# Performance work log

Hardware: AMD Instinct MI355X
Metric: run time of the kernel (lower is better)

The kernel has to match this reference:

```python
import jax, jax.numpy as jnp
import numpy as np

N = 50000
E = 800000
NUM_GRAPHS = 128
X_IN, HID, EDGE_DIM = 64, 64, 16


def setup_inputs() -> dict:
    key = jax.random.key(0)
    ks = jax.random.split(key, 9)
    s = 0.05
    inp = {
        'x': jax.random.normal(ks[0], (N, X_IN), jnp.float32),
        'edge_index': jax.random.randint(ks[1], (2, E), 0, N, dtype=jnp.int32),
        'edge_attr': jax.random.normal(ks[2], (E, EDGE_DIM), jnp.float32),
        'batch': jnp.sort(jax.random.randint(ks[3], (N,), 0, NUM_GRAPHS, dtype=jnp.int32)),
        'w_fc1': jax.random.normal(ks[4], (EDGE_DIM, 1), jnp.float32) * s,
        'b_fc1': jnp.zeros((1,), jnp.float32),
    }
    dims = [(X_IN, HID), (HID, HID * 2), (HID * 2, HID)]
    for i, (din, dout) in enumerate(dims):
        k1, k2, k3 = jax.random.split(ks[5 + i], 3)
        inp[f'w1_{i}'] = jax.random.normal(k1, (din, dout), jnp.float32) * s
        inp[f'b1_{i}'] = jnp.zeros((dout,), jnp.float32)
        inp[f'w2_{i}'] = jax.random.normal(k2, (din, dout), jnp.float32) * s
        inp[f'w3_{i}'] = jax.random.normal(k3, (din, dout), jnp.float32) * s
        inp[f'b3_{i}'] = jnp.zeros((dout,), jnp.float32)
    return inp


def leconv(x, src, dst, ew, w1, b1, w2, w3, b3):
    # PyG LEConv: out_i = lin3(x_i) + sum_{j->i} e_ji * (lin1(x_j) - lin2(x_i))
    a = x @ w1 + b1          # lin1 (bias=True)   [N, out]
    b = x @ w2               # lin2 (bias=False)  [N, out]
    msg = ew[:, None] * (a[src] - b[dst])          # [E, out]
    agg = jax.ops.segment_sum(msg, dst, num_segments=N)
    return agg + x @ w3 + b3  # lin3 (bias=True)


def reference(x, edge_index, edge_attr, batch,
              w_fc1, b_fc1,
              w1_0, b1_0, w2_0, w3_0, b3_0,
              w1_1, b1_1, w2_1, w3_1, b3_1,
              w1_2, b1_2, w2_2, w3_2, b3_2):
    src, dst = edge_index[0], edge_index[1]
    ew = (edge_attr @ w_fc1 + b_fc1)[:, 0]         # fc1(edge_attr).squeeze(-1) -> [E]
    h = jax.nn.elu(leconv(x, src, dst, ew, w1_0, b1_0, w2_0, w3_0, b3_0))
    h = jax.nn.elu(leconv(h, src, dst, ew, w1_1, b1_1, w2_1, w3_1, b3_1))
    h = jax.nn.elu(leconv(h, src, dst, ew, w1_2, b1_2, w2_2, w3_2, b3_2))
    # global max pool over nodes of each graph -> [NUM_GRAPHS, HID]
    return jax.ops.segment_max(h, batch, num_segments=NUM_GRAPHS)
```

## Files before the change

### kernel.cpp

```cpp
#include <hip/hip_runtime.h>
#include <math.h>

#define N_NODES 50000
#define N_EDGES 800000
#define NUM_GRAPHS_ 128
#define SCAN_NB 98
#define NPASS 8
#define NODES_PER_PASS 6250
#define HCHUNKS 128
#define EDGES_PER_CHUNK 6250
#define HWORDS 12500

typedef unsigned short u16;
typedef unsigned int u32;
typedef __attribute__((ext_vector_type(8))) short bf16x8;
typedef __attribute__((ext_vector_type(4))) float f32x4;

__device__ __forceinline__ float elu_f(float v) {
    return v > 0.f ? v : (__expf(v) - 1.f);
}
__device__ __forceinline__ u16 f2bf(float f) {
    u32 u = __float_as_uint(f);
    u += 0x7FFFu + ((u >> 16) & 1u);
    return (u16)(u >> 16);
}
__device__ __forceinline__ float bf2f(u16 h) {
    return __uint_as_float(((u32)h) << 16);
}
__device__ __forceinline__ void bfpair(u32 v, float& lo, float& hi) {
    lo = __uint_as_float(v << 16);
    hi = __uint_as_float(v & 0xFFFF0000u);
}
__device__ __forceinline__ u32 packbf(float lo, float hi) {
    return (u32)f2bf(lo) | ((u32)f2bf(hi) << 16);
}

__global__ void conv_x_kernel(const float* __restrict__ x, u16* __restrict__ xb) {
    int g = blockIdx.x * blockDim.x + threadIdx.x;
    float4 v = ((const float4*)x)[g];
    uint2 o;
    o.x = packbf(v.x, v.y);
    o.y = packbf(v.z, v.w);
    ((uint2*)xb)[g] = o;
}

__global__ void ew_kernel(const float* __restrict__ edge_attr,
                          const float* __restrict__ w_fc1,
                          const float* __restrict__ b_fc1,
                          const int* __restrict__ edge_index,
                          float* __restrict__ ew,
                          u16* __restrict__ dst16) {
    int e = blockIdx.x * blockDim.x + threadIdx.x;
    if (e >= N_EDGES) return;
    const float4* ea = (const float4*)(edge_attr + (size_t)e * 16);
    const float4* wf = (const float4*)w_fc1;
    float acc = b_fc1[0];
#pragma unroll
    for (int i = 0; i < 4; i++) {
        float4 a = ea[i], w = wf[i];
        acc += a.x * w.x + a.y * w.y + a.z * w.z + a.w * w.w;
    }
    ew[e] = acc;
    dst16[e] = (u16)edge_index[N_EDGES + e];
}

__global__ __launch_bounds__(256) void deg_hist_kernel(const u16* __restrict__ dst16,
                                                       u32* __restrict__ partial) {
    __shared__ u32 bins[HWORDS];
    const int c = blockIdx.x >> 1;
    const int p = blockIdx.x & 1;
    const int t = threadIdx.x;
    for (int i = t; i < HWORDS; i += 256) bins[i] = 0;
    __syncthreads();
    const int base = c * EDGES_PER_CHUNK;
    const int nlo = p * 25000;
    for (int i = t; i < EDGES_PER_CHUNK; i += 256) {
        const int b = (int)dst16[base + i] - nlo;
        if ((unsigned)b < 25000u)
            atomicAdd(&bins[b >> 1], 1u << ((b & 1) * 16));
    }
    __syncthreads();
    u32* outp = partial + (size_t)blockIdx.x * HWORDS;
    for (int i = t; i < HWORDS; i += 256) outp[i] = bins[i];
}

__global__ __launch_bounds__(256) void scan_chunks_kernel(const u32* __restrict__ partial,
                                                          u32* __restrict__ prefpack,
                                                          u32* __restrict__ degpack) {
    const int g = blockIdx.x * 256 + threadIdx.x;
    if (g >= 25000) return;
    const int p = (g >= HWORDS) ? 1 : 0;
    const int wh = g - p * HWORDS;
    u32 runlo = 0, runhi = 0;
    for (int c = 0; c < HCHUNKS; c++) {
        prefpack[(size_t)c * 25000 + g] = runlo | (runhi << 16);
        u32 v = partial[(size_t)((c << 1) + p) * HWORDS + wh];
        runlo += v & 0xFFFFu;
        runhi += v >> 16;
    }
    degpack[g] = runlo | (runhi << 16);
}

__global__ __launch_bounds__(256) void scan1_kernel(const u32* __restrict__ degpack,
                                                    int* __restrict__ rowptr,
                                                    int* __restrict__ blk_sums) {
    __shared__ int sh[256];
    const int t = threadIdx.x;
    const int base = blockIdx.x * 512;
    const int i0 = base + 2 * t, i1 = i0 + 1;
    int d0 = 0, d1 = 0;
    if (i0 < N_NODES) {
        u32 v = degpack[i0 >> 1];
        d0 = (int)(v & 0xFFFFu);
        d1 = (int)(v >> 16);
    }
    const int pair = d0 + d1;
    int v = pair;
    sh[t] = v;
    __syncthreads();
#pragma unroll
    for (int off = 1; off < 256; off <<= 1) {
        int add = (t >= off) ? sh[t - off] : 0;
        __syncthreads();
        v += add;
        sh[t] = v;
        __syncthreads();
    }
    const int excl = v - pair;
    if (i0 < N_NODES) rowptr[i0] = excl;
    if (i1 < N_NODES) rowptr[i1] = excl + d0;
    if (t == 255) blk_sums[blockIdx.x] = v;
}

__global__ __launch_bounds__(128) void scan2_kernel(const int* __restrict__ blk_sums,
                                                    int* __restrict__ blk_offs,
                                                    int* __restrict__ rowptr) {
    __shared__ int sh[128];
    const int t = threadIdx.x;
    const int orig = (t < SCAN_NB) ? blk_sums[t] : 0;
    int v = orig;
    sh[t] = v;
    __syncthreads();
#pragma unroll
    for (int off = 1; off < 128; off <<= 1) {
        int add = (t >= off) ? sh[t - off] : 0;
        __syncthreads();
        v += add;
        sh[t] = v;
        __syncthreads();
    }
    if (t < SCAN_NB) blk_offs[t] = v - orig;
    if (t == 127) rowptr[N_NODES] = v;
}

__global__ void scan3_kernel(int* __restrict__ rowptr,
                             const int* __restrict__ blk_offs) {
    int i = blockIdx.x * blockDim.x + threadIdx.x;
    if (i >= N_NODES) return;
    rowptr[i] += blk_offs[i >> 9];
}

__global__ __launch_bounds__(256) void place_kernel(const int* __restrict__ edge_index,
                                                    const float* __restrict__ ew,
                                                    const u16* __restrict__ dst16,
                                                    const int* __restrict__ rowptr,
                                                    const u32* __restrict__ prefpack,
                                                    int2* __restrict__ csr) {
    __shared__ int lcur[NODES_PER_PASS];
    const int pass = blockIdx.x & (NPASS - 1);
    const int c = blockIdx.x >> 3;
    const int lo = pass * NODES_PER_PASS;
    const int t = threadIdx.x;
    for (int i = t; i < NODES_PER_PASS; i += 256) lcur[i] = 0;
    __syncthreads();
    const int base = c * EDGES_PER_CHUNK;
    for (int i = t; i < EDGES_PER_CHUNK; i += 256) {
        const int e = base + i;
        const int d = (int)dst16[e];
        const int dl = d - lo;
        if ((unsigned)dl < (unsigned)NODES_PER_PASS) {
            u32 pw = prefpack[(size_t)c * 25000 + (d >> 1)];
            int pref = (int)((pw >> ((d & 1) * 16)) & 0xFFFFu);
            int lpos = atomicAdd(&lcur[dl], 1);
            int2 ent;
            ent.x = edge_index[e];
            ent.y = __float_as_int(ew[e]);
            csr[rowptr[d] + pref + lpos] = ent;
        }
    }
}

template <int DIN, bool WRITE_C>
__global__ __launch_bounds__(256) void gather_kernel(
    const u16* __restrict__ xb, const int* __restrict__ rowptr,
    const int2* __restrict__ csr, u16* __restrict__ sb,
    u16* __restrict__ chb, float* __restrict__ c) {
    constexpr int CG = DIN / 4;
    constexpr int EG = 64 / CG;
    const int gid = blockIdx.x * 256 + threadIdx.x;
    const int node = gid >> 6;
    if (node >= N_NODES) return;
    const int lane = threadIdx.x & 63;
    const int cg = lane & (CG - 1);
    const int eg = lane / CG;
    const int beg = rowptr[node];
    const int end = rowptr[node + 1];
    const uint2* x2 = (const uint2*)xb;

    float a0 = 0.f, a1 = 0.f, a2 = 0.f, a3 = 0.f;
    float b0 = 0.f, b1 = 0.f, b2 = 0.f, b3 = 0.f;
    float wsum = 0.f;

    int p = beg + eg;
    for (; p + EG < end; p += 2 * EG) {
        int2 e0 = csr[p];
        int2 e1 = csr[p + EG];
        float w0 = __int_as_float(e0.y);
        float w1 = __int_as_float(e1.y);
        uint2 v0 = x2[(size_t)e0.x * CG + cg];
        uint2 v1 = x2[(size_t)e1.x * CG + cg];
        float f0, f1, f2, f3, g0, g1, g2, g3;
        bfpair(v0.x, f0, f1); bfpair(v0.y, f2, f3);
        bfpair(v1.x, g0, g1); bfpair(v1.y, g2, g3);
        a0 += w0 * f0; a1 += w0 * f1; a2 += w0 * f2; a3 += w0 * f3;
        b0 += w1 * g0; b1 += w1 * g1; b2 += w1 * g2; b3 += w1 * g3;
        wsum += w0 + w1;
    }
    if (p < end) {
        int2 e0 = csr[p];
        float w0 = __int_as_float(e0.y);
        uint2 v0 = x2[(size_t)e0.x * CG + cg];
        float f0, f1, f2, f3;
        bfpair(v0.x, f0, f1); bfpair(v0.y, f2, f3);
        a0 += w0 * f0; a1 += w0 * f1; a2 += w0 * f2; a3 += w0 * f3;
        wsum += w0;
    }
    a0 += b0; a1 += b1; a2 += b2; a3 += b3;

#pragma unroll
    for (int off = 32; off >= CG; off >>= 1) {
        a0 += __shfl_xor(a0, off);
        a1 += __shfl_xor(a1, off);
        a2 += __shfl_xor(a2, off);
        a3 += __shfl_xor(a3, off);
        wsum += __shfl_xor(wsum, off);
    }

    if (lane < CG) {
        uint2 so;
        so.x = packbf(a0, a1);
        so.y = packbf(a2, a3);
        ((uint2*)sb)[(size_t)node * CG + cg] = so;
        const float cn = WRITE_C ? wsum : c[node];
        uint2 hv = x2[(size_t)node * CG + cg];
        float h0, h1, h2, h3;
        bfpair(hv.x, h0, h1); bfpair(hv.y, h2, h3);
        uint2 co;
        co.x = packbf(cn * h0, cn * h1);
        co.y = packbf(cn * h2, cn * h3);
        ((uint2*)chb)[(size_t)node * CG + cg] = co;
    }
    if (WRITE_C && lane == 0) c[node] = wsum;
}

__global__ void pack_w_kernel(const float* __restrict__ w3_0, const float* __restrict__ w1_0, const float* __restrict__ w2_0,
                              const float* __restrict__ w3_1, const float* __restrict__ w1_1, const float* __restrict__ w2_1,
                              const float* __restrict__ w3_2, const float* __restrict__ w1_2, const float* __restrict__ w2_2,
                              u16* __restrict__ bp0, u16* __restrict__ bp1, u16* __restrict__ bp2) {
    int t = blockIdx.x * blockDim.x + threadIdx.x;
    if (t >= 7680) return;
    u16 buf[8];
    if (t < 4608) {
        int DIN, DOUT, lid;
        const float *w3, *w1, *w2;
        u16* bp;
        if (t < 1536) { DIN = 64; DOUT = 64;  lid = t;        w3 = w3_0; w1 = w1_0; w2 = w2_0; bp = bp0; }
        else          { DIN = 64; DOUT = 128; lid = t - 1536; w3 = w3_1; w1 = w1_1; w2 = w2_1; bp = bp1; }
        const int NT = DOUT / 16;
        const int lane = lid & 63;
        const int fragid = lid >> 6;
        const int chunk = fragid / NT;
        const int ntile = fragid % NT;
        const int n = ntile * 16 + (lane & 15);
        const int kbase = chunk * 32 + (lane >> 4) * 8;
#pragma unroll
        for (int j = 0; j < 8; j++) {
            int k = kbase + j;
            int region = k / DIN;
            int kk = k - region * DIN;
            float v = (region == 0) ? w3[kk * DOUT + n]
                    : (region == 1) ? w1[kk * DOUT + n]
                                    : -w2[kk * DOUT + n];
            buf[j] = f2bf(v);
        }
        *(bf16x8*)(bp + ((size_t)lid << 3)) = *(bf16x8*)buf;
    } else {
        const int lid = t - 4608;
        const int NT = 12;
        const int lane = lid & 63;
        const int fragid = lid >> 6;
        const int chunk = fragid / NT;
        const int ntile = fragid % NT;
        const int n = ntile * 16 + (lane & 15);
        const int kbase = chunk * 32 + (lane >> 4) * 8;
#pragma unroll
        for (int j = 0; j < 8; j++) {
            int k = kbase + j;
            float v = (n < 64)  ? w3_2[k * 64 + n]
                    : (n < 128) ? -w2_2[k * 64 + (n - 64)]
                                : w1_2[k * 64 + (n - 128)];
            buf[j] = f2bf(v);
        }
        *(bf16x8*)(bp2 + ((size_t)lid << 3)) = *(bf16x8*)buf;
    }
}

template <int DIN, int DOUT>
__global__ __launch_bounds__(256) void gemm_mfma(
    const u16* __restrict__ hb, const u16* __restrict__ sb,
    const u16* __restrict__ chb, const u16* __restrict__ Bp,
    const float* __restrict__ cvec, const float* __restrict__ bias1,
    const float* __restrict__ bias3, u16* __restrict__ outp) {
    constexpr int CH = DIN / 32;
    constexpr int CHUNKS = 3 * CH;
    constexpr int NT = DOUT / 16;
    const int tid = threadIdx.x;
    const int wv = tid >> 6;
    const int lane = tid & 63;
    const int l15 = lane & 15;
    const int q = lane >> 4;
    const int mhalf = wv & 1;
    const int nhalf = wv >> 1;
    const int row_base = blockIdx.x * 64 + mhalf * 32;
    const int nt0 = blockIdx.y * 4 + nhalf * 2;

    const int r0 = min(row_base + l15, N_NODES - 1);
    const int r1 = min(row_base + 16 + l15, N_NODES - 1);
    const int qo = q * 8;

    f32x4 acc00 = {0.f, 0.f, 0.f, 0.f};
    f32x4 acc01 = {0.f, 0.f, 0.f, 0.f};
    f32x4 acc10 = {0.f, 0.f, 0.f, 0.f};
    f32x4 acc11 = {0.f, 0.f, 0.f, 0.f};

#pragma unroll
    for (int chunk = 0; chunk < CHUNKS; chunk++) {
        const int region = chunk / CH;
        const int koff = (chunk - region * CH) * 32 + qo;
        const u16* A = (region == 0) ? hb : (region == 1) ? sb : chb;
        bf16x8 a0 = *(const bf16x8*)(A + (size_t)r0 * DIN + koff);
        bf16x8 a1 = *(const bf16x8*)(A + (size_t)r1 * DIN + koff);
        const u16* bp = Bp + (((size_t)(chunk * NT + nt0) * 64 + lane) << 3);
        bf16x8 bf0 = *(const bf16x8*)bp;
        bf16x8 bf1 = *(const bf16x8*)(bp + 64 * 8);
        acc00 = __builtin_amdgcn_mfma_f32_16x16x32_bf16(a0, bf0, acc00, 0, 0, 0);
        acc01 = __builtin_amdgcn_mfma_f32_16x16x32_bf16(a0, bf1, acc01, 0, 0, 0);
        acc10 = __builtin_amdgcn_mfma_f32_16x16x32_bf16(a1, bf0, acc10, 0, 0, 0);
        acc11 = __builtin_amdgcn_mfma_f32_16x16x32_bf16(a1, bf1, acc11, 0, 0, 0);
    }

#pragma unroll
    for (int ni = 0; ni < 2; ni++) {
        const int col = (nt0 + ni) * 16 + l15;
        const float B3 = bias3[col];
        const float B1 = bias1[col];
        const f32x4 am0 = ni ? acc01 : acc00;
        const f32x4 am1 = ni ? acc11 : acc10;
#pragma unroll
        for (int mi = 0; mi < 2; mi++) {
            const f32x4 av = mi ? am1 : am0;
#pragma unroll
            for (int reg = 0; reg < 4; reg++) {
                const int row = row_base + mi * 16 + q * 4 + reg;
                if (row < N_NODES) {
                    const float cv = cvec[row];
                    const float val = av[reg] + B3 + cv * B1;
                    outp[(size_t)row * DOUT + col] = f2bf(elu_f(val));
                }
            }
        }
    }
}

__global__ __launch_bounds__(256) void gemm_wide_kernel(
    const u16* __restrict__ hb, const u16* __restrict__ Bp,
    u16* __restrict__ zuy) {
    constexpr int NT = 12;
    const int tid = threadIdx.x;
    const int wv = tid >> 6;
    const int lane = tid & 63;
    const int l15 = lane & 15;
    const int q = lane >> 4;
    const int row_base = blockIdx.x * 64 + (wv & 1) * 32;
    const int nt0 = blockIdx.y * 4 + (wv >> 1) * 2;

    const int r0 = min(row_base + l15, N_NODES - 1);
    const int r1 = min(row_base + 16 + l15, N_NODES - 1);
    const int qo = q * 8;

    f32x4 acc00 = {0.f, 0.f, 0.f, 0.f};
    f32x4 acc01 = {0.f, 0.f, 0.f, 0.f};
    f32x4 acc10 = {0.f, 0.f, 0.f, 0.f};
    f32x4 acc11 = {0.f, 0.f, 0.f, 0.f};

#pragma unroll
    for (int chunk = 0; chunk < 4; chunk++) {
        const int koff = chunk * 32 + qo;
        bf16x8 a0 = *(const bf16x8*)(hb + (size_t)r0 * 128 + koff);
        bf16x8 a1 = *(const bf16x8*)(hb + (size_t)r1 * 128 + koff);
        const u16* bp = Bp + (((size_t)(chunk * NT + nt0) * 64 + lane) << 3);
        bf16x8 bf0 = *(const bf16x8*)bp;
        bf16x8 bf1 = *(const bf16x8*)(bp + 64 * 8);
        acc00 = __builtin_amdgcn_mfma_f32_16x16x32_bf16(a0, bf0, acc00, 0, 0, 0);
        acc01 = __builtin_amdgcn_mfma_f32_16x16x32_bf16(a0, bf1, acc01, 0, 0, 0);
        acc10 = __builtin_amdgcn_mfma_f32_16x16x32_bf16(a1, bf0, acc10, 0, 0, 0);
        acc11 = __builtin_amdgcn_mfma_f32_16x16x32_bf16(a1, bf1, acc11, 0, 0, 0);
    }

#pragma unroll
    for (int ni = 0; ni < 2; ni++) {
        const int col = (nt0 + ni) * 16 + l15;
        const f32x4 am0 = ni ? acc01 : acc00;
        const f32x4 am1 = ni ? acc11 : acc10;
#pragma unroll
        for (int mi = 0; mi < 2; mi++) {
            const f32x4 av = mi ? am1 : am0;
#pragma unroll
            for (int reg = 0; reg < 4; reg++) {
                const int row = row_base + mi * 16 + q * 4 + reg;
                if (row < N_NODES)
                    zuy[(size_t)row * 192 + col] = f2bf(av[reg]);
            }
        }
    }
}

__global__ __launch_bounds__(256) void gather2_kernel(
    const u16* __restrict__ zuy, const int* __restrict__ rowptr,
    const int2* __restrict__ csr, const float* __restrict__ c,
    const float* __restrict__ bias1, const float* __restrict__ bias3,
    u16* __restrict__ h3) {
    constexpr int CG = 16, EG = 4;
    const int gid = blockIdx.x * 256 + threadIdx.x;
    const int node = gid >> 6;
    if (node >= N_NODES) return;
    const int lane = threadIdx.x & 63;
    const int cg = lane & (CG - 1);
    const int eg = lane >> 4;
    const int beg = rowptr[node];
    const int end = rowptr[node + 1];

    float a0 = 0.f, a1 = 0.f, a2 = 0.f, a3 = 0.f;
    float b0 = 0.f, b1 = 0.f, b2 = 0.f, b3 = 0.f;

    int p = beg + eg;
    for (; p + EG < end; p += 2 * EG) {
        int2 e0 = csr[p];
        int2 e1 = csr[p + EG];
        float w0 = __int_as_float(e0.y);
        float w1 = __int_as_float(e1.y);
        uint2 v0 = ((const uint2*)(zuy + (size_t)e0.x * 192 + 128))[cg];
        uint2 v1 = ((const uint2*)(zuy + (size_t)e1.x * 192 + 128))[cg];
        float f0, f1, f2, f3, g0, g1, g2, g3;
        bfpair(v0.x, f0, f1); bfpair(v0.y, f2, f3);
        bfpair(v1.x, g0, g1); bfpair(v1.y, g2, g3);
        a0 += w0 * f0; a1 += w0 * f1; a2 += w0 * f2; a3 += w0 * f3;
        b0 += w1 * g0; b1 += w1 * g1; b2 += w1 * g2; b3 += w1 * g3;
    }
    if (p < end) {
        int2 e0 = csr[p];
        float w0 = __int_as_float(e0.y);
        uint2 v0 = ((const uint2*)(zuy + (size_t)e0.x * 192 + 128))[cg];
        float f0, f1, f2, f3;
        bfpair(v0.x, f0, f1); bfpair(v0.y, f2, f3);
        a0 += w0 * f0; a1 += w0 * f1; a2 += w0 * f2; a3 += w0 * f3;
    }
    a0 += b0; a1 += b1; a2 += b2; a3 += b3;

#pragma unroll
    for (int off = 32; off >= CG; off >>= 1) {
        a0 += __shfl_xor(a0, off);
        a1 += __shfl_xor(a1, off);
        a2 += __shfl_xor(a2, off);
        a3 += __shfl_xor(a3, off);
    }

    if (lane < CG) {
        const float cn = c[node];
        const u16* zr = zuy + (size_t)node * 192;
        uint2 zv = ((const uint2*)zr)[cg];
        uint2 uv = ((const uint2*)(zr + 64))[cg];
        float z0, z1, z2, z3, u0, u1, u2, u3;
        bfpair(zv.x, z0, z1); bfpair(zv.y, z2, z3);
        bfpair(uv.x, u0, u1); bfpair(uv.y, u2, u3);
        const float4 b3v = *(const float4*)(bias3 + cg * 4);
        const float4 b1v = *(const float4*)(bias1 + cg * 4);
        float o0 = elu_f(z0 + cn * u0 + a0 + b3v.x + cn * b1v.x);
        float o1 = elu_f(z1 + cn * u1 + a1 + b3v.y + cn * b1v.y);
        float o2 = elu_f(z2 + cn * u2 + a2 + b3v.z + cn * b1v.z);
        float o3 = elu_f(z3 + cn * u3 + a3 + b3v.w + cn * b1v.w);
        uint2 o;
        o.x = packbf(o0, o1);
        o.y = packbf(o2, o3);
        ((uint2*)h3)[(size_t)node * CG + cg] = o;
    }
}

__global__ void pool_kernel(const u16* __restrict__ h,
                            const int* __restrict__ batch,
                            float* __restrict__ out) {
    const int g = blockIdx.x;
    const int tid = threadIdx.x;
    int lo = 0, hi = N_NODES;
    while (lo < hi) { int mid = (lo + hi) >> 1; if (batch[mid] < g) lo = mid + 1; else hi = mid; }
    const int beg = lo;
    lo = beg; hi = N_NODES;
    while (lo < hi) { int mid = (lo + hi) >> 1; if (batch[mid] < g + 1) lo = mid + 1; else hi = mid; }
    const int end = lo;

    __shared__ float red[256];
    const int col = tid & 63;
    const int rg = tid >> 6;
    float m = -3.0e38f;
    for (int r = beg + rg; r < end; r += 4) m = fmaxf(m, bf2f(h[(size_t)r * 64 + col]));
    red[tid] = m;
    __syncthreads();
    if (tid < 64) {
        m = fmaxf(fmaxf(red[tid], red[tid + 64]), fmaxf(red[tid + 128], red[tid + 192]));
        out[g * 64 + tid] = m;
    }
}

extern "C" void kernel_launch(void* const* d_in, const int* in_sizes, int n_in,
                              void* d_out, int out_size, void* d_ws, size_t ws_size,
                              hipStream_t stream) {
    const float* x = (const float*)d_in[0];
    const int* ei = (const int*)d_in[1];
    const float* ea = (const float*)d_in[2];
    const int* batch = (const int*)d_in[3];
    const float* wfc = (const float*)d_in[4];
    const float* bfc = (const float*)d_in[5];
    const float* w1_0 = (const float*)d_in[6];
    const float* b1_0 = (const float*)d_in[7];
    const float* w2_0 = (const float*)d_in[8];
    const float* w3_0 = (const float*)d_in[9];
    const float* b3_0 = (const float*)d_in[10];
    const float* w1_1 = (const float*)d_in[11];
    const float* b1_1 = (const float*)d_in[12];
    const float* w2_1 = (const float*)d_in[13];
    const float* w3_1 = (const float*)d_in[14];
    const float* b3_1 = (const float*)d_in[15];
    const float* w1_2 = (const float*)d_in[16];
    const float* b1_2 = (const float*)d_in[17];
    const float* w2_2 = (const float*)d_in[18];
    const float* w3_2 = (const float*)d_in[19];
    const float* b3_2 = (const float*)d_in[20];
    float* out = (float*)d_out;

    char* ws = (char*)d_ws;
    float* ew      = (float*)(ws);
    float* c       = (float*)(ws + 3200000);
    int*   rowptr  = (int*)  (ws + 3800000);
    int2*  csr     = (int2*) (ws + 4000128);
    u16*   xb      = (u16*)  (ws + 10400128);
    u16*   sb      = (u16*)  (ws + 16800128);
    u16*   chb     = (u16*)  (ws + 29600128);
    u16*   h1      = (u16*)  (ws + 42400128);
    u16*   h2      = (u16*)  (ws + 48800128);
    u16*   h3      = (u16*)  (ws + 61600128);
    u16*   bp0     = (u16*)  (ws + 68000128);
    u16*   bp1     = (u16*)  (ws + 68024704);
    u16*   bp2     = (u16*)  (ws + 68073856);
    int* blk_sums  = (int*)  (ws + 68123008);
    int* blk_offs  = (int*)  (ws + 68123520);
    u16* dst16   = chb;
    u32* degpack = (u32*)(ws + 31600128);
    u32* partial = (u32*)sb;
    u32* prefpack = (u32*)h2;
    u16* zuy     = sb;

    conv_x_kernel<<<3125, 256, 0, stream>>>(x, xb);
    ew_kernel<<<(N_EDGES + 255) / 256, 256, 0, stream>>>(ea, wfc, bfc, ei, ew, dst16);
    pack_w_kernel<<<30, 256, 0, stream>>>(w3_0, w1_0, w2_0, w3_1, w1_1, w2_1,
                                          w3_2, w1_2, w2_2, bp0, bp1, bp2);
    deg_hist_kernel<<<HCHUNKS * 2, 256, 0, stream>>>(dst16, partial);
    scan_chunks_kernel<<<98, 256, 0, stream>>>(partial, prefpack, degpack);
    scan1_kernel<<<SCAN_NB, 256, 0, stream>>>(degpack, rowptr, blk_sums);
    scan2_kernel<<<1, 128, 0, stream>>>(blk_sums, blk_offs, rowptr);
    scan3_kernel<<<(N_NODES + 255) / 256, 256, 0, stream>>>(rowptr, blk_offs);
    place_kernel<<<HCHUNKS * NPASS, 256, 0, stream>>>(ei, ew, dst16, rowptr, prefpack, csr);

    const int RB = (N_NODES + 63) / 64;
    const int GBLK = (N_NODES * 64 + 255) / 256;

    gather_kernel<64, true><<<GBLK, 256, 0, stream>>>(xb, rowptr, csr, sb, chb, c);
    gemm_mfma<64, 64><<<dim3(RB, 1), 256, 0, stream>>>(xb, sb, chb, bp0, c, b1_0, b3_0, h1);

    gather_kernel<64, false><<<GBLK, 256, 0, stream>>>(h1, rowptr, csr, sb, chb, c);
    gemm_mfma<64, 128><<<dim3(RB, 2), 256, 0, stream>>>(h1, sb, chb, bp1, c, b1_1, b3_1, h2);

    gemm_wide_kernel<<<dim3(RB, 3), 256, 0, stream>>>(h2, bp2, zuy);
    gather2_kernel<<<GBLK, 256, 0, stream>>>(zuy, rowptr, csr, c, b1_2, b3_2, h3);

    pool_kernel<<<NUM_GRAPHS_, 256, 0, stream>>>(h3, batch, out);
}
```

Before: 350.0 us.

## Replace deterministic chunked CSR build with global-atomic degree count and placement

Replaces the shared-memory chunked histogram, multi-stage scan and stable chunked placement with global atomic degree counting in the edge-weight kernel, a single-block 1024-thread scan, and per-edge atomic slot placement. This cuts several kernel launches and the large partial/prefix buffers. The cost is global atomic contention on 50k counters, a serial single-block scan, and a nondeterministic edge order within each row, so the floating-point summation order becomes nondeterministic.

Result: slower. 488.2 us (+39.5%).

```diff
diff --git a/kernel.cpp b/kernel.cpp
--- a/kernel.cpp
+++ b/kernel.cpp
@@ -4,12 +4,6 @@
 #define N_NODES 50000
 #define N_EDGES 800000
 #define NUM_GRAPHS_ 128
-#define SCAN_NB 98
-#define NPASS 8
-#define NODES_PER_PASS 6250
-#define HCHUNKS 128
-#define EDGES_PER_CHUNK 6250
-#define HWORDS 12500
 
 typedef unsigned short u16;
 typedef unsigned int u32;
@@ -35,8 +29,10 @@
     return (u32)f2bf(lo) | ((u32)f2bf(hi) << 16);
 }
 
-__global__ void conv_x_kernel(const float* __restrict__ x, u16* __restrict__ xb) {
+__global__ void conv_x_kernel(const float* __restrict__ x, u16* __restrict__ xb,
+                              int4* __restrict__ deg4) {
     int g = blockIdx.x * blockDim.x + threadIdx.x;
+    if (g < N_NODES / 4) deg4[g] = (int4){0, 0, 0, 0};
     float4 v = ((const float4*)x)[g];
     uint2 o;
     o.x = packbf(v.x, v.y);
@@ -49,7 +45,7 @@
                           const float* __restrict__ b_fc1,
                           const int* __restrict__ edge_index,
                           float* __restrict__ ew,
-                          u16* __restrict__ dst16) {
+                          int* __restrict__ deg) {
     int e = blockIdx.x * blockDim.x + threadIdx.x;
     if (e >= N_EDGES) return;
     const float4* ea = (const float4*)(edge_attr + (size_t)e * 16);
@@ -61,133 +57,60 @@
         acc += a.x * w.x + a.y * w.y + a.z * w.z + a.w * w.w;
     }
     ew[e] = acc;
-    dst16[e] = (u16)edge_index[N_EDGES + e];
-}
-
-__global__ __launch_bounds__(256) void deg_hist_kernel(const u16* __restrict__ dst16,
-                                                       u32* __restrict__ partial) {
-    __shared__ u32 bins[HWORDS];
-    const int c = blockIdx.x >> 1;
-    const int p = blockIdx.x & 1;
+    atomicAdd(&deg[edge_index[N_EDGES + e]], 1);
+}
+
+#define SCAN_T 1024
+#define SCAN_CHUNK 49
+
+__global__ __launch_bounds__(1024) void scan_kernel(const int* __restrict__ deg,
+                                                    int* __restrict__ rowptr,
+                                                    int* __restrict__ cur) {
+    __shared__ int sh[SCAN_T];
     const int t = threadIdx.x;
-    for (int i = t; i < HWORDS; i += 256) bins[i] = 0;
-    __syncthreads();
-    const int base = c * EDGES_PER_CHUNK;
-    const int nlo = p * 25000;
-    for (int i = t; i < EDGES_PER_CHUNK; i += 256) {
-        const int b = (int)dst16[base + i] - nlo;
-        if ((unsigned)b < 25000u)
-            atomicAdd(&bins[b >> 1], 1u << ((b & 1) * 16));
-    }
-    __syncthreads();
-    u32* outp = partial + (size_t)blockIdx.x * HWORDS;
-    for (int i = t; i < HWORDS; i += 256) outp[i] = bins[i];
-}
-
-__global__ __launch_bounds__(256) void scan_chunks_kernel(const u32* __restrict__ partial,
-                                                          u32* __restrict__ prefpack,
-                                                          u32* __restrict__ degpack) {
-    const int g = blockIdx.x * 256 + threadIdx.x;
-    if (g >= 25000) return;
-    const int p = (g >= HWORDS) ? 1 : 0;
-    const int wh = g - p * HWORDS;
-    u32 runlo = 0, runhi = 0;
-    for (int c = 0; c < HCHUNKS; c++) {
-        prefpack[(size_t)c * 25000 + g] = runlo | (runhi << 16);
-        u32 v = partial[(size_t)((c << 1) + p) * HWORDS + wh];
-        runlo += v & 0xFFFFu;
-        runhi += v >> 16;
-    }
-    degpack[g] = runlo | (runhi << 16);
-}
-
-__global__ __launch_bounds__(256) void scan1_kernel(const u32* __restrict__ degpack,
-                                                    int* __restrict__ rowptr,
-                                                    int* __restrict__ blk_sums) {
-    __shared__ int sh[256];
-    const int t = threadIdx.x;
-    const int base = blockIdx.x * 512;
-    const int i0 = base + 2 * t, i1 = i0 + 1;
-    int d0 = 0, d1 = 0;
-    if (i0 < N_NODES) {
-        u32 v = degpack[i0 >> 1];
-        d0 = (int)(v & 0xFFFFu);
-        d1 = (int)(v >> 16);
-    }
-    const int pair = d0 + d1;
-    int v = pair;
+    const int base = t * SCAN_CHUNK;
+    int s = 0;
+#pragma unroll
+    for (int i = 0; i < SCAN_CHUNK; i++) {
+        const int idx = base + i;
+        if (idx < N_NODES) s += deg[idx];
+    }
+    int v = s;
     sh[t] = v;
     __syncthreads();
 #pragma unroll
-    for (int off = 1; off < 256; off <<= 1) {
+    for (int off = 1; off < SCAN_T; off <<= 1) {
         int add = (t >= off) ? sh[t - off] : 0;
         __syncthreads();
         v += add;
         sh[t] = v;
         __syncthreads();
     }
-    const int excl = v - pair;
-    if (i0 < N_NODES) rowptr[i0] = excl;
-    if (i1 < N_NODES) rowptr[i1] = excl + d0;
-    if (t == 255) blk_sums[blockIdx.x] = v;
-}
-
-__global__ __launch_bounds__(128) void scan2_kernel(const int* __restrict__ blk_sums,
-                                                    int* __restrict__ blk_offs,
-                                                    int* __restrict__ rowptr) {
-    __shared__ int sh[128];
-    const int t = threadIdx.x;
-    const int orig = (t < SCAN_NB) ? blk_sums[t] : 0;
-    int v = orig;
-    sh[t] = v;
-    __syncthreads();
-#pragma unroll
-    for (int off = 1; off < 128; off <<= 1) {
-        int add = (t >= off) ? sh[t - off] : 0;
-        __syncthreads();
-        v += add;
-        sh[t] = v;
-        __syncthreads();
-    }
-    if (t < SCAN_NB) blk_offs[t] = v - orig;
-    if (t == 127) rowptr[N_NODES] = v;
-}
-
-__global__ void scan3_kernel(int* __restrict__ rowptr,
-                             const int* __restrict__ blk_offs) {
-    int i = blockIdx.x * blockDim.x + threadIdx.x;
-    if (i >= N_NODES) return;
-    rowptr[i] += blk_offs[i >> 9];
+    int run = v - s;
+#pragma unroll
+    for (int i = 0; i < SCAN_CHUNK; i++) {
+        const int idx = base + i;
+        if (idx < N_NODES) {
+            rowptr[idx] = run;
+            cur[idx] = run;
+            run += deg[idx];
+        }
+    }
+    if (t == SCAN_T - 1) rowptr[N_NODES] = v;
 }
 
 __global__ __launch_bounds__(256) void place_kernel(const int* __restrict__ edge_index,
                                                     const float* __restrict__ ew,
-                                                    const u16* __restrict__ dst16,
-                                                    const int* __restrict__ rowptr,
-                                                    const u32* __restrict__ prefpack,
+                                                    int* __restrict__ cur,
                                                     int2* __restrict__ csr) {
-    __shared__ int lcur[NODES_PER_PASS];
-    const int pass = blockIdx.x & (NPASS - 1);
-    const int c = blockIdx.x >> 3;
-    const int lo = pass * NODES_PER_PASS;
-    const int t = threadIdx.x;
-    for (int i = t; i < NODES_PER_PASS; i += 256) lcur[i] = 0;
-    __syncthreads();
-    const int base = c * EDGES_PER_CHUNK;
-    for (int i = t; i < EDGES_PER_CHUNK; i += 256) {
-        const int e = base + i;
-        const int d = (int)dst16[e];
-        const int dl = d - lo;
-        if ((unsigned)dl < (unsigned)NODES_PER_PASS) {
-            u32 pw = prefpack[(size_t)c * 25000 + (d >> 1)];
-            int pref = (int)((pw >> ((d & 1) * 16)) & 0xFFFFu);
-            int lpos = atomicAdd(&lcur[dl], 1);
-            int2 ent;
-            ent.x = edge_index[e];
-            ent.y = __float_as_int(ew[e]);
-            csr[rowptr[d] + pref + lpos] = ent;
-        }
-    }
+    const int e = blockIdx.x * 256 + threadIdx.x;
+    if (e >= N_EDGES) return;
+    const int d = edge_index[N_EDGES + e];
+    const int slot = atomicAdd(&cur[d], 1);
+    int2 ent;
+    ent.x = edge_index[e];
+    ent.y = __float_as_int(ew[e]);
+    csr[slot] = ent;
 }
 
 template <int DIN, bool WRITE_C>
@@ -571,24 +494,16 @@
     u16*   bp0     = (u16*)  (ws + 68000128);
     u16*   bp1     = (u16*)  (ws + 68024704);
     u16*   bp2     = (u16*)  (ws + 68073856);
-    int* blk_sums  = (int*)  (ws + 68123008);
-    int* blk_offs  = (int*)  (ws + 68123520);
-    u16* dst16   = chb;
-    u32* degpack = (u32*)(ws + 31600128);
-    u32* partial = (u32*)sb;
-    u32* prefpack = (u32*)h2;
-    u16* zuy     = sb;
-
-    conv_x_kernel<<<3125, 256, 0, stream>>>(x, xb);
-    ew_kernel<<<(N_EDGES + 255) / 256, 256, 0, stream>>>(ea, wfc, bfc, ei, ew, dst16);
+    int*   deg     = (int*)  (ws + 68123008);
+    int*   cur     = (int*)  (ws + 68323008);
+    u16* zuy = sb;
+
+    conv_x_kernel<<<3125, 256, 0, stream>>>(x, xb, (int4*)deg);
+    ew_kernel<<<3125, 256, 0, stream>>>(ea, wfc, bfc, ei, ew, deg);
     pack_w_kernel<<<30, 256, 0, stream>>>(w3_0, w1_0, w2_0, w3_1, w1_1, w2_1,
                                           w3_2, w1_2, w2_2, bp0, bp1, bp2);
-    deg_hist_kernel<<<HCHUNKS * 2, 256, 0, stream>>>(dst16, partial);
-    scan_chunks_kernel<<<98, 256, 0, stream>>>(partial, prefpack, degpack);
-    scan1_kernel<<<SCAN_NB, 256, 0, stream>>>(degpack, rowptr, blk_sums);
-    scan2_kernel<<<1, 128, 0, stream>>>(blk_sums, blk_offs, rowptr);
-    scan3_kernel<<<(N_NODES + 255) / 256, 256, 0, stream>>>(rowptr, blk_offs);
-    place_kernel<<<HCHUNKS * NPASS, 256, 0, stream>>>(ei, ew, dst16, rowptr, prefpack, csr);
+    scan_kernel<<<1, SCAN_T, 0, stream>>>(deg, rowptr, cur);
+    place_kernel<<<3125, 256, 0, stream>>>(ei, ew, cur, csr);
 
     const int RB = (N_NODES + 63) / 64;
     const int GBLK = (N_NODES * 64 + 255) / 256;
```

## Fuse layer-1 GEMM with layer-2 wide GEMM through shared memory

Applied to the files above, without the earlier changes.

Combines the second LEConv GEMM (with bias, c-scaling and ELU) and the following wide projection GEMM into one kernel. The intermediate 64x128 h2 tile stays in LDS instead of going to global memory, which removes the h2 write and reread plus one launch. Each block now covers all output columns, so the grid is smaller (RB blocks rather than RB×2 and RB×3) and each thread holds more accumulators, which may lower parallelism and occupancy. Workspace buffers are reassigned so that h3 reuses xb.

Result: faster. 337.5 us (-3.6%).

```diff
diff --git a/kernel.cpp b/kernel.cpp
--- a/kernel.cpp
+++ b/kernel.cpp
@@ -382,54 +382,87 @@
     }
 }
 
-__global__ __launch_bounds__(256) void gemm_wide_kernel(
-    const u16* __restrict__ hb, const u16* __restrict__ Bp,
+__global__ __launch_bounds__(256) void gemm_l1_fused(
+    const u16* __restrict__ hb, const u16* __restrict__ sb,
+    const u16* __restrict__ chb, const u16* __restrict__ Bp1,
+    const u16* __restrict__ Bp2, const float* __restrict__ cvec,
+    const float* __restrict__ bias1, const float* __restrict__ bias3,
     u16* __restrict__ zuy) {
-    constexpr int NT = 12;
+    __shared__ u16 ht[64][136];
     const int tid = threadIdx.x;
     const int wv = tid >> 6;
     const int lane = tid & 63;
     const int l15 = lane & 15;
     const int q = lane >> 4;
-    const int row_base = blockIdx.x * 64 + (wv & 1) * 32;
-    const int nt0 = blockIdx.y * 4 + (wv >> 1) * 2;
-
+    const int mhalf = wv & 1;
+    const int nhalf = wv >> 1;
+    const int row_base = blockIdx.x * 64 + mhalf * 32;
     const int r0 = min(row_base + l15, N_NODES - 1);
     const int r1 = min(row_base + 16 + l15, N_NODES - 1);
     const int qo = q * 8;
 
-    f32x4 acc00 = {0.f, 0.f, 0.f, 0.f};
-    f32x4 acc01 = {0.f, 0.f, 0.f, 0.f};
-    f32x4 acc10 = {0.f, 0.f, 0.f, 0.f};
-    f32x4 acc11 = {0.f, 0.f, 0.f, 0.f};
-
-#pragma unroll
-    for (int chunk = 0; chunk < 4; chunk++) {
-        const int koff = chunk * 32 + qo;
-        bf16x8 a0 = *(const bf16x8*)(hb + (size_t)r0 * 128 + koff);
-        bf16x8 a1 = *(const bf16x8*)(hb + (size_t)r1 * 128 + koff);
-        const u16* bp = Bp + (((size_t)(chunk * NT + nt0) * 64 + lane) << 3);
-        bf16x8 bf0 = *(const bf16x8*)bp;
-        bf16x8 bf1 = *(const bf16x8*)(bp + 64 * 8);
-        acc00 = __builtin_amdgcn_mfma_f32_16x16x32_bf16(a0, bf0, acc00, 0, 0, 0);
-        acc01 = __builtin_amdgcn_mfma_f32_16x16x32_bf16(a0, bf1, acc01, 0, 0, 0);
-        acc10 = __builtin_amdgcn_mfma_f32_16x16x32_bf16(a1, bf0, acc10, 0, 0, 0);
-        acc11 = __builtin_amdgcn_mfma_f32_16x16x32_bf16(a1, bf1, acc11, 0, 0, 0);
-    }
-
-#pragma unroll
-    for (int ni = 0; ni < 2; ni++) {
-        const int col = (nt0 + ni) * 16 + l15;
-        const f32x4 am0 = ni ? acc01 : acc00;
-        const f32x4 am1 = ni ? acc11 : acc10;
-#pragma unroll
-        for (int mi = 0; mi < 2; mi++) {
-            const f32x4 av = mi ? am1 : am0;
-#pragma unroll
-            for (int reg = 0; reg < 4; reg++) {
-                const int row = row_base + mi * 16 + q * 4 + reg;
-                if (row < N_NODES)
-                    zuy[(size_t)row * 192 + col] = f2bf(av[reg]);
+    {
+        const int nt0 = nhalf * 4;
+        f32x4 acc[2][4] = {};
+#pragma unroll
+        for (int chunk = 0; chunk < 6; chunk++) {
+            const int region = chunk / 2;
+            const int koff = (chunk - region * 2) * 32 + qo;
+            const u16* A = (region == 0) ? hb : (region == 1) ? sb : chb;
+            bf16x8 a0 = *(const bf16x8*)(A + (size_t)r0 * 64 + koff);
+            bf16x8 a1 = *(const bf16x8*)(A + (size_t)r1 * 64 + koff);
+#pragma unroll
+            for (int ni = 0; ni < 4; ni++) {
+                bf16x8 bf = *(const bf16x8*)(Bp1 + (((size_t)(chunk * 8 + nt0 + ni) * 64 + lane) << 3));
+                acc[0][ni] = __builtin_amdgcn_mfma_f32_16x16x32_bf16(a0, bf, acc[0][ni], 0, 0, 0);
+                acc[1][ni] = __builtin_amdgcn_mfma_f32_16x16x32_bf16(a1, bf, acc[1][ni], 0, 0, 0);
+            }
+        }
+#pragma unroll
+        for (int ni = 0; ni < 4; ni++) {
+            const int col = (nt0 + ni) * 16 + l15;
+            const float B3 = bias3[col];
+            const float B1 = bias1[col];
+#pragma unroll
+            for (int mi = 0; mi < 2; mi++) {
+#pragma unroll
+                for (int reg = 0; reg < 4; reg++) {
+                    const int lrow = mhalf * 32 + mi * 16 + q * 4 + reg;
+                    const int grow = blockIdx.x * 64 + lrow;
+                    const float cv = cvec[min(grow, N_NODES - 1)];
+                    ht[lrow][col] = f2bf(elu_f(acc[mi][ni][reg] + B3 + cv * B1));
+                }
+            }
+        }
+    }
+    __syncthreads();
+
+    {
+        const int nt2 = nhalf * 6;
+        f32x4 acc[2][6] = {};
+#pragma unroll
+        for (int chunk = 0; chunk < 4; chunk++) {
+            const int koff = chunk * 32 + qo;
+            bf16x8 a0 = *(const bf16x8*)(&ht[mhalf * 32 + l15][koff]);
+            bf16x8 a1 = *(const bf16x8*)(&ht[mhalf * 32 + 16 + l15][koff]);
+#pragma unroll
+            for (int ni = 0; ni < 6; ni++) {
+                bf16x8 bf = *(const bf16x8*)(Bp2 + (((size_t)(chunk * 12 + nt2 + ni) * 64 + lane) << 3));
+                acc[0][ni] = __builtin_amdgcn_mfma_f32_16x16x32_bf16(a0, bf, acc[0][ni], 0, 0, 0);
+                acc[1][ni] = __builtin_amdgcn_mfma_f32_16x16x32_bf16(a1, bf, acc[1][ni], 0, 0, 0);
+            }
+        }
+#pragma unroll
+        for (int ni = 0; ni < 6; ni++) {
+            const int col = (nt2 + ni) * 16 + l15;
+#pragma unroll
+            for (int mi = 0; mi < 2; mi++) {
+#pragma unroll
+                for (int reg = 0; reg < 4; reg++) {
+                    const int row = row_base + mi * 16 + q * 4 + reg;
+                    if (row < N_NODES)
+                        zuy[(size_t)row * 192 + col] = f2bf(acc[mi][ni][reg]);
+                }
             }
         }
     }
@@ -566,8 +599,7 @@
     u16*   sb      = (u16*)  (ws + 16800128);
     u16*   chb     = (u16*)  (ws + 29600128);
     u16*   h1      = (u16*)  (ws + 42400128);
-    u16*   h2      = (u16*)  (ws + 48800128);
-    u16*   h3      = (u16*)  (ws + 61600128);
+    u16*   zuy     = (u16*)  (ws + 48800128);
     u16*   bp0     = (u16*)  (ws + 68000128);
     u16*   bp1     = (u16*)  (ws + 68024704);
     u16*   bp2     = (u16*)  (ws + 68073856);
@@ -576,8 +608,8 @@
     u16* dst16   = chb;
     u32* degpack = (u32*)(ws + 31600128);
     u32* partial = (u32*)sb;
-    u32* prefpack = (u32*)h2;
-    u16* zuy     = sb;
+    u32* prefpack = (u32*)zuy;
+    u16* h3 = xb;
 
     conv_x_kernel<<<3125, 256, 0, stream>>>(x, xb);
     ew_kernel<<<(N_EDGES + 255) / 256, 256, 0, stream>>>(ea, wfc, bfc, ei, ew, dst16);
@@ -597,9 +629,8 @@
     gemm_mfma<64, 64><<<dim3(RB, 1), 256, 0, stream>>>(xb, sb, chb, bp0, c, b1_0, b3_0, h1);
 
     gather_kernel<64, false><<<GBLK, 256, 0, stream>>>(h1, rowptr, csr, sb, chb, c);
-    gemm_mfma<64, 128><<<dim3(RB, 2), 256, 0, stream>>>(h1, sb, chb, bp1, c, b1_1, b3_1, h2);
-
-    gemm_wide_kernel<<<dim3(RB, 3), 256, 0, stream>>>(h2, bp2, zuy);
+    gemm_l1_fused<<<RB, 256, 0, stream>>>(h1, sb, chb, bp1, bp2, c, b1_1, b3_1, zuy);
+
     gather2_kernel<<<GBLK, 256, 0, stream>>>(zuy, rowptr, csr, c, b1_2, b3_2, h3);
 
     pool_kernel<<<NUM_GRAPHS_, 256, 0, stream>>>(h3, batch, out);
```
